# Performance work log

Measured on AMD Instinct MI355X. Metric: run time of the kernel, lower is better.

Reference implementation:

```python
import jax, jax.numpy as jnp
import numpy as np

NUM_HEADS = 4
LOCAL_RADIUS = 2


def setup_inputs() -> dict:
    key = jax.random.key(0)
    ks = jax.random.split(key, 7)
    B, C, H, W = 1, 256, 40, 40
    O = 256  # out_channels
    s = 1.0 / np.sqrt(C).astype(np.float32)
    x = jax.random.normal(ks[0], (B, C, H, W), dtype=jnp.float32)
    Wq = jax.random.normal(ks[1], (C, O), dtype=jnp.float32) * s
    Wk = jax.random.normal(ks[2], (C, O), dtype=jnp.float32) * s
    Wv = jax.random.normal(ks[3], (C, O), dtype=jnp.float32) * s
    bq = jnp.zeros((O,), jnp.float32)
    bk = jnp.zeros((O,), jnp.float32)
    bv = jnp.zeros((O,), jnp.float32)
    return {"x": x, "Wq": Wq, "bq": bq, "Wk": Wk, "bk": bk, "Wv": Wv, "bv": bv}


def reference(x, Wq, bq, Wk, bk, Wv, bv):
    B, C, H, W = x.shape
    N = H * W
    O = Wq.shape[1]
    hd = O // NUM_HEADS
    # Faithful to torch: x.view(B, N, -1) is a raw row-major reshape of (B,C,H,W)
    xf = x.reshape(B, N, C)
    # projections -> (B, heads, N, head_dim)
    q = (xf @ Wq + bq).reshape(B, N, NUM_HEADS, hd).transpose(0, 2, 1, 3)
    k = (xf @ Wk + bk).reshape(B, N, NUM_HEADS, hd).transpose(0, 2, 1, 3)
    v = (xf @ Wv + bv).reshape(B, N, NUM_HEADS, hd).transpose(0, 2, 1, 3)
    scale = jnp.asarray(O, jnp.float32) ** 0.5
    acc = jnp.zeros_like(v)
    # 25 shifted full-attention passes; roll is over (heads, points) axes,
    # exactly matching torch key.roll(shifts=(h,w), dims=(-3,-2)).
    for h in range(-LOCAL_RADIUS, LOCAL_RADIUS + 1):
        for w in range(-LOCAL_RADIUS, LOCAL_RADIUS + 1):
            rk = jnp.roll(k, shift=(h, w), axis=(1, 2))
            scores = jnp.einsum('bhnd,bhmd->bhnm', q, rk) / scale  # (B,h,N,N)
            attn = jax.nn.softmax(scores, axis=-1)
            rv = jnp.roll(v, shift=(-h, -w), axis=(1, 2))
            acc = acc + jnp.einsum('bhnm,bhmd->bhnd', attn, rv)
    # (B, heads, N, hd) -> (B, N, O)
    return acc.transpose(0, 2, 1, 3).reshape(B, N, O)
```

## Files before the change

### kernel.cpp

```cpp
#include <hip/hip_runtime.h>
#include <hip/hip_bf16.h>
#include <stdint.h>

typedef __attribute__((ext_vector_type(8))) __bf16 bf16x8;
typedef __attribute__((ext_vector_type(4))) float f32x4;

#define N_PTS 1600
#define HD    64

#define OFF_XC   0u
#define OFF_WT   819200u
#define OFF_BIAS 1212416u
#define OFF_VHT  1213952u
#define OFF_QH   2033152u
#define OFF_KH   2852352u
#define OFF_KF   0u
#define OFF_OP   2852352u
#define OFF_LP   9405952u
#define OFF_VF   9610752u

__device__ __forceinline__ float bf2f(ushort h) {
  union { uint32_t u; float f; } v; v.u = ((uint32_t)h) << 16; return v.f;
}
__device__ __forceinline__ ushort f2bf(float f) {
  union { float f; uint32_t u; } v; v.f = f;
  uint32_t u = v.u;
  return (ushort)((u + 0x7FFFu + ((u >> 16) & 1u)) >> 16);
}
__device__ __forceinline__ uint32_t pk2(float a, float b) {
  union { __hip_bfloat162 h; uint32_t u; } cv;
  cv.h = __float22bfloat162_rn(make_float2(a, b));
  return cv.u;
}

__device__ __forceinline__ int detect_f32(const ushort* xu, int* shflag) {
  int t = threadIdx.x & 255;
  if (t == 0) *shflag = 0;
  __syncthreads();
  int local = 0;
#pragma unroll
  for (int i = 0; i < 4; ++i) {
    float v = bf2f(xu[(t * 4 + i) * 2]);
    if (!(fabsf(v) < 1e4f)) local = 1;
  }
  if (local) atomicOr(shflag, 1);
  __syncthreads();
  return *shflag;
}

__global__ void k_prep(const void* __restrict__ x, const void* __restrict__ Wq,
                       const void* __restrict__ bq, const void* __restrict__ Wk,
                       const void* __restrict__ bk, const void* __restrict__ Wv,
                       const void* __restrict__ bv, char* __restrict__ ws) {
  __shared__ int shflag;
  __shared__ ushort tileb[32][33];
  int isf32 = detect_f32((const ushort*)x, &shflag);
  int b = blockIdx.x, t = threadIdx.x;

  if (b < 400) {
    ushort4 o;
    if (isf32) {
      float4 f = ((const float4*)x)[b * 256 + t];
      o.x = f2bf(f.x); o.y = f2bf(f.y); o.z = f2bf(f.z); o.w = f2bf(f.w);
    } else {
      o = ((const ushort4*)x)[b * 256 + t];
    }
    ((ushort4*)(ws + OFF_XC))[b * 256 + t] = o;
  } else if (b < 592) {
    int w = b - 400, z = w >> 6, tile = w & 63;
    const void* W = (z == 0) ? Wq : ((z == 1) ? Wk : Wv);
    int o0 = (tile & 7) * 32, k0 = (tile >> 3) * 32;
    int tx = t & 31, ty = t >> 5;
#pragma unroll
    for (int i = 0; i < 32; i += 8) {
      int kk = (k0 + ty + i) * 256 + o0 + tx;
      tileb[ty + i][tx] = isf32 ? f2bf(((const float*)W)[kk]) : ((const ushort*)W)[kk];
    }
    __syncthreads();
    ushort* WT = (ushort*)(ws + OFF_WT) + z * 65536;
#pragma unroll
    for (int i = 0; i < 32; i += 8)
      WT[(o0 + ty + i) * 256 + k0 + tx] = tileb[tx][ty + i];
  } else {
    ushort* bb = (ushort*)(ws + OFF_BIAS);
#pragma unroll
    for (int z = 0; z < 3; ++z) {
      const void* B = (z == 0) ? bq : ((z == 1) ? bk : bv);
      bb[z * 256 + t] = isf32 ? f2bf(((const float*)B)[t]) : ((const ushort*)B)[t];
    }
  }
}

__launch_bounds__(256)
__global__ void k_proj(const ushort* __restrict__ X, const ushort* __restrict__ WT,
                       const ushort* __restrict__ bias3,
                       ushort* __restrict__ Qh, ushort* __restrict__ Kh, ushort* __restrict__ VhT) {
  int z = blockIdx.z;
  const ushort* WTz = WT + z * 65536;
  const ushort* bias = bias3 + z * 256;
  int n0 = blockIdx.x * 16;
  int head = threadIdx.x >> 6;
  int lane = threadIdx.x & 63;
  int c = lane & 15, quad = lane >> 4;

  f32x4 acc[4];
#pragma unroll
  for (int i = 0; i < 4; ++i) acc[i] = (f32x4){0.f, 0.f, 0.f, 0.f};

  const ushort* xrow = X + (n0 + c) * 256;
#pragma unroll
  for (int kt = 0; kt < 8; ++kt) {
    bf16x8 a = *(const bf16x8*)(xrow + kt * 32 + quad * 8);
#pragma unroll
    for (int os = 0; os < 4; ++os) {
      bf16x8 bfr = *(const bf16x8*)(WTz + (head * 64 + os * 16 + c) * 256 + kt * 32 + quad * 8);
      acc[os] = __builtin_amdgcn_mfma_f32_16x16x32_bf16(a, bfr, acc[os], 0, 0, 0);
    }
  }
  if (z == 2) {
#pragma unroll
    for (int os = 0; os < 4; ++os) {
      float bval = bf2f(bias[head * 64 + os * 16 + c]);
      ushort4 v;
      v.x = f2bf(acc[os][0] + bval); v.y = f2bf(acc[os][1] + bval);
      v.z = f2bf(acc[os][2] + bval); v.w = f2bf(acc[os][3] + bval);
      *(ushort4*)(VhT + (head * 64 + os * 16 + c) * N_PTS + n0 + quad * 4) = v;
    }
  } else {
    float scale = (z == 0) ? 0.0625f * 1.44269504088896f : 1.0f;
    ushort* out = (z == 0) ? Qh : Kh;
#pragma unroll
    for (int os = 0; os < 4; ++os) {
      float bval = bf2f(bias[head * 64 + os * 16 + c]);
#pragma unroll
      for (int r = 0; r < 4; ++r)
        out[head * (N_PTS * HD) + (n0 + quad * 4 + r) * HD + os * 16 + c] =
            f2bf((acc[os][r] + bval) * scale);
    }
  }
}

__global__ void k_frag(const ushort* __restrict__ Kh, const ushort* __restrict__ VhT,
                       ushort* __restrict__ Kf, ushort* __restrict__ Vf) {
  int q = blockIdx.x * 256 + threadIdx.x;
  int isV = q >= 51200;
  int idx = isV ? q - 51200 : q;
  int lane = idx & 63, ch = (idx >> 6) & 3;
  int rest = idx >> 8;
  int t = rest % 50, g = rest / 50;
  int c = lane & 15, quad = lane >> 4;
  if (!isV) {
    int perm = ((c >> 2) << 3) + (c & 3);
    int key = t * 32 + perm + ((ch >> 1) << 2);
    int d0 = (ch & 1) * 32 + quad * 8;
    bf16x8 v = *(const bf16x8*)(Kh + (size_t)(g * N_PTS + key) * HD + d0);
    *(bf16x8*)(Kf + (size_t)idx * 8) = v;
  } else {
    int d = ch * 16 + c;
    int m0 = t * 32 + quad * 8;
    const ushort* row = VhT + (size_t)(g * HD + d) * N_PTS;
    int mp = (m0 == 0) ? 1592 : m0 - 8;
    int mn = (m0 == 1592) ? 0 : m0 + 8;
    union { bf16x8 v[3]; ushort us[24]; } w;
    w.v[0] = *(const bf16x8*)(row + mp);
    w.v[1] = *(const bf16x8*)(row + m0);
    w.v[2] = *(const bf16x8*)(row + mn);
    union { ushort us[8]; bf16x8 v; } o;
#pragma unroll
    for (int j = 0; j < 8; ++j) {
      float s = bf2f(w.us[4 + j]) + bf2f(w.us[6 + j]) + bf2f(w.us[8 + j]) +
                bf2f(w.us[10 + j]) + bf2f(w.us[12 + j]);
      o.us[j] = f2bf(s);
    }
    *(bf16x8*)(Vf + (size_t)idx * 8) = o.v;
  }
}

__device__ __forceinline__ bf16x8 pack_p8(const f32x4& s0, const f32x4& s1, float& lp) {
  float e0 = exp2f(s0[0]), e1 = exp2f(s0[1]), e2 = exp2f(s0[2]), e3 = exp2f(s0[3]);
  float e4 = exp2f(s1[0]), e5 = exp2f(s1[1]), e6 = exp2f(s1[2]), e7 = exp2f(s1[3]);
  lp += ((e0 + e1) + (e2 + e3)) + ((e4 + e5) + (e6 + e7));
  union { uint32_t u[4]; bf16x8 v; } r;
  r.u[0] = pk2(e0, e1); r.u[1] = pk2(e2, e3);
  r.u[2] = pk2(e4, e5); r.u[3] = pk2(e6, e7);
  return r.v;
}

__launch_bounds__(256, 4)
__global__ void k_attn(const ushort* __restrict__ Qh, const ushort* __restrict__ Kf,
                       const ushort* __restrict__ Vf, ushort* __restrict__ Opart,
                       float* __restrict__ Lpart) {
  int qt = blockIdx.x;
  int yy = blockIdx.y;
  int z  = blockIdx.z;
  int hp = yy >> 2, kg = yy & 3;
  int vg = (2 * hp - kg + 8) & 3;
  int tid = threadIdx.x, sp = tid >> 6, lane = tid & 63;
  int c = lane & 15, quad = lane >> 4;
  int n0 = qt * 16;

  __shared__ float obuf[4][16][68];
  __shared__ float lbuf[4][16];

  const ushort* q0row = Qh + ((hp    ) * N_PTS + n0 + c) * HD;
  const ushort* q1row = Qh + ((hp + 2) * N_PTS + n0 + c) * HD;
  bf16x8 qa00 = *(const bf16x8*)(q0row + quad * 8);
  bf16x8 qa01 = *(const bf16x8*)(q0row + 32 + quad * 8);
  bf16x8 qa10 = *(const bf16x8*)(q1row + quad * 8);
  bf16x8 qa11 = *(const bf16x8*)(q1row + 32 + quad * 8);

  f32x4 oacc0[4], oacc1[4];
#pragma unroll
  for (int i = 0; i < 4; ++i) {
    oacc0[i] = (f32x4){0.f, 0.f, 0.f, 0.f};
    oacc1[i] = (f32x4){0.f, 0.f, 0.f, 0.f};
  }
  float lp0 = 0.f, lp1 = 0.f;

  int off = (sp == 0) ? 0 : (sp == 1) ? 7 : (sp == 2) ? 13 : 19;
  int iters = (sp == 0) ? 7 : 6;
  int t0 = z * 25 + off;
  const f32x4 z4 = (f32x4){0.f, 0.f, 0.f, 0.f};

  const char* kfp = (const char*)Kf + (size_t)(kg * 50 + t0) * 4096 + lane * 16;
  const char* vfp = (const char*)Vf + (size_t)(vg * 50 + t0) * 4096 + lane * 16;

  for (int it = 0; it < iters; ++it) {
    const char* kt = kfp + it * 4096;
    const char* vt = vfp + it * 4096;
    bf16x8 ka0 = *(const bf16x8*)(kt);
    bf16x8 ka1 = *(const bf16x8*)(kt + 1024);
    bf16x8 kb0 = *(const bf16x8*)(kt + 2048);
    bf16x8 kb1 = *(const bf16x8*)(kt + 3072);
    bf16x8 vb[4];
#pragma unroll
    for (int ds = 0; ds < 4; ++ds)
      vb[ds] = *(const bf16x8*)(vt + ds * 1024);

    f32x4 s0 = __builtin_amdgcn_mfma_f32_16x16x32_bf16(ka0, qa00, z4, 0, 0, 0);
    s0 = __builtin_amdgcn_mfma_f32_16x16x32_bf16(ka1, qa01, s0, 0, 0, 0);
    f32x4 s1 = __builtin_amdgcn_mfma_f32_16x16x32_bf16(kb0, qa00, z4, 0, 0, 0);
    s1 = __builtin_amdgcn_mfma_f32_16x16x32_bf16(kb1, qa01, s1, 0, 0, 0);
    bf16x8 pa = pack_p8(s0, s1, lp0);
#pragma unroll
    for (int ds = 0; ds < 4; ++ds)
      oacc0[ds] = __builtin_amdgcn_mfma_f32_16x16x32_bf16(pa, vb[ds], oacc0[ds], 0, 0, 0);

    s0 = __builtin_amdgcn_mfma_f32_16x16x32_bf16(ka0, qa10, z4, 0, 0, 0);
    s0 = __builtin_amdgcn_mfma_f32_16x16x32_bf16(ka1, qa11, s0, 0, 0, 0);
    s1 = __builtin_amdgcn_mfma_f32_16x16x32_bf16(kb0, qa10, z4, 0, 0, 0);
    s1 = __builtin_amdgcn_mfma_f32_16x16x32_bf16(kb1, qa11, s1, 0, 0, 0);
    bf16x8 pa1 = pack_p8(s0, s1, lp1);
#pragma unroll
    for (int ds = 0; ds < 4; ++ds)
      oacc1[ds] = __builtin_amdgcn_mfma_f32_16x16x32_bf16(pa1, vb[ds], oacc1[ds], 0, 0, 0);
  }

  lp0 += __shfl_xor(lp0, 16, 64); lp0 += __shfl_xor(lp0, 32, 64);
  lp1 += __shfl_xor(lp1, 16, 64); lp1 += __shfl_xor(lp1, 32, 64);

#pragma unroll
  for (int h = 0; h < 2; ++h) {
    __syncthreads();
    const f32x4* oa = h ? oacc1 : oacc0;
#pragma unroll
    for (int ds = 0; ds < 4; ++ds)
#pragma unroll
      for (int r = 0; r < 4; ++r)
        obuf[sp][quad * 4 + r][ds * 16 + c] = oa[ds][r];
    if (quad == 0) lbuf[sp][c] = h ? lp1 : lp0;
    __syncthreads();

    int q = tid >> 4, d0 = (tid & 15) * 4;
    f32x4 a = *(const f32x4*)&obuf[0][q][d0];
    a += *(const f32x4*)&obuf[1][q][d0];
    a += *(const f32x4*)&obuf[2][q][d0];
    a += *(const f32x4*)&obuf[3][q][d0];
    float l = lbuf[0][q] + lbuf[1][q] + lbuf[2][q] + lbuf[3][q];
    int hq = hp + 2 * h;
    union { uint32_t u[2]; } wv;
    wv.u[0] = pk2(a[0], a[1]);
    wv.u[1] = pk2(a[2], a[3]);
    *(uint2*)&Opart[(size_t)((z * 4 + kg) * N_PTS + n0 + q) * 256 + hq * 64 + d0] =
        *(uint2*)wv.u;
    if ((tid & 15) == 0)
      Lpart[((z * 4 + kg) * 4 + hq) * N_PTS + n0 + q] = l;
  }
}

__global__ void k_out(const ushort* __restrict__ Opart, const float* __restrict__ Lpart,
                      const void* __restrict__ x, void* __restrict__ out) {
  __shared__ int shflag;
  int isf32 = detect_f32((const ushort*)x, &shflag);
  int idx = blockIdx.x * 256 + threadIdx.x;
  int n = idx >> 8, o = idx & 255, hq = o >> 6;
  float acc = 0.f;
#pragma unroll
  for (int kg = 0; kg < 4; ++kg) {
    float num = bf2f(Opart[(size_t)((0 + kg) * N_PTS + n) * 256 + o]) +
                bf2f(Opart[(size_t)((4 + kg) * N_PTS + n) * 256 + o]);
    float l = Lpart[((0 + kg) * 4 + hq) * N_PTS + n] +
              Lpart[((4 + kg) * 4 + hq) * N_PTS + n];
    float w = (kg == ((hq + 2) & 3)) ? 2.f : 1.f;
    acc += w * num / l;
  }
  if (isf32) ((float*)out)[idx] = acc;
  else       ((ushort*)out)[idx] = f2bf(acc);
}

extern "C" void kernel_launch(void* const* d_in, const int* in_sizes, int n_in,
                              void* d_out, int out_size, void* d_ws, size_t ws_size,
                              hipStream_t stream) {
  char* ws = (char*)d_ws;
  ushort* Xc    = (ushort*)(ws + OFF_XC);
  ushort* WT    = (ushort*)(ws + OFF_WT);
  ushort* bias3 = (ushort*)(ws + OFF_BIAS);
  ushort* VhT   = (ushort*)(ws + OFF_VHT);
  ushort* Qh    = (ushort*)(ws + OFF_QH);
  ushort* Kh    = (ushort*)(ws + OFF_KH);
  ushort* Kf    = (ushort*)(ws + OFF_KF);
  ushort* Vf    = (ushort*)(ws + OFF_VF);
  ushort* Opart = (ushort*)(ws + OFF_OP);
  float*  Lpart = (float*)(ws + OFF_LP);

  k_prep<<<593, 256, 0, stream>>>(d_in[0], d_in[1], d_in[2], d_in[3],
                                  d_in[4], d_in[5], d_in[6], ws);
  k_proj<<<dim3(100, 1, 3), 256, 0, stream>>>(Xc, WT, bias3, Qh, Kh, VhT);
  k_frag<<<400, 256, 0, stream>>>(Kh, VhT, Kf, Vf);
  k_attn<<<dim3(100, 8, 2), 256, 0, stream>>>(Qh, Kf, Vf, Opart, Lpart);
  k_out<<<1600, 256, 0, stream>>>(Opart, Lpart, d_in[0], d_out);
}
```

Measured before the change: 113.0 us.

## Merge key-split grid dimension and double-buffer K/V fragment loads in attention

Removes the z split of the key range, so each block's four waves now cover all 50 key tiles, and halves the partial outputs that k_out must reduce. The inner loop is rewritten with two register sets (A/B), so the next tile's K/V fragments are loaded while the current tile's MFMAs run. The MFMA sections are wrapped in s_setprio, and the launch_bounds occupancy hint is dropped. The grid shrinks from 1600 to 800 blocks and register pressure rises, which may reduce occupancy and latency hiding.

```diff
diff --git a/kernel.cpp b/kernel.cpp
--- a/kernel.cpp
+++ b/kernel.cpp
@@ -186,13 +186,50 @@
   return r.v;
 }
 
-__launch_bounds__(256, 4)
+#define MFMA16(a, b, cc) __builtin_amdgcn_mfma_f32_16x16x32_bf16(a, b, cc, 0, 0, 0)
+
+#define LOADT(sfx, t) do {                                            \
+    const char* kt_ = kfp + (size_t)(t) * 4096;                       \
+    const char* vt_ = vfp + (size_t)(t) * 4096;                       \
+    ka0##sfx = *(const bf16x8*)(kt_);                                 \
+    ka1##sfx = *(const bf16x8*)(kt_ + 1024);                          \
+    kb0##sfx = *(const bf16x8*)(kt_ + 2048);                          \
+    kb1##sfx = *(const bf16x8*)(kt_ + 3072);                          \
+    vb0##sfx = *(const bf16x8*)(vt_);                                 \
+    vb1##sfx = *(const bf16x8*)(vt_ + 1024);                          \
+    vb2##sfx = *(const bf16x8*)(vt_ + 2048);                          \
+    vb3##sfx = *(const bf16x8*)(vt_ + 3072);                          \
+  } while (0)
+
+#define COMPUTE(sfx) do {                                             \
+    __builtin_amdgcn_s_setprio(1);                                    \
+    f32x4 s0 = MFMA16(ka0##sfx, qa00, z4);                            \
+    s0 = MFMA16(ka1##sfx, qa01, s0);                                  \
+    f32x4 s1 = MFMA16(kb0##sfx, qa00, z4);                            \
+    s1 = MFMA16(kb1##sfx, qa01, s1);                                  \
+    bf16x8 pa0 = pack_p8(s0, s1, lp0);                                \
+    oacc0[0] = MFMA16(pa0, vb0##sfx, oacc0[0]);                       \
+    oacc0[1] = MFMA16(pa0, vb1##sfx, oacc0[1]);                       \
+    oacc0[2] = MFMA16(pa0, vb2##sfx, oacc0[2]);                       \
+    oacc0[3] = MFMA16(pa0, vb3##sfx, oacc0[3]);                       \
+    s0 = MFMA16(ka0##sfx, qa10, z4);                                  \
+    s0 = MFMA16(ka1##sfx, qa11, s0);                                  \
+    s1 = MFMA16(kb0##sfx, qa10, z4);                                  \
+    s1 = MFMA16(kb1##sfx, qa11, s1);                                  \
+    bf16x8 pa1 = pack_p8(s0, s1, lp1);                                \
+    oacc1[0] = MFMA16(pa1, vb0##sfx, oacc1[0]);                       \
+    oacc1[1] = MFMA16(pa1, vb1##sfx, oacc1[1]);                       \
+    oacc1[2] = MFMA16(pa1, vb2##sfx, oacc1[2]);                       \
+    oacc1[3] = MFMA16(pa1, vb3##sfx, oacc1[3]);                       \
+    __builtin_amdgcn_s_setprio(0);                                    \
+  } while (0)
+
+__launch_bounds__(256)
 __global__ void k_attn(const ushort* __restrict__ Qh, const ushort* __restrict__ Kf,
                        const ushort* __restrict__ Vf, ushort* __restrict__ Opart,
                        float* __restrict__ Lpart) {
   int qt = blockIdx.x;
   int yy = blockIdx.y;
-  int z  = blockIdx.z;
   int hp = yy >> 2, kg = yy & 3;
   int vg = (2 * hp - kg + 8) & 3;
   int tid = threadIdx.x, sp = tid >> 6, lane = tid & 63;
@@ -217,44 +254,26 @@
   }
   float lp0 = 0.f, lp1 = 0.f;
 
-  int off = (sp == 0) ? 0 : (sp == 1) ? 7 : (sp == 2) ? 13 : 19;
-  int iters = (sp == 0) ? 7 : 6;
-  int t0 = z * 25 + off;
+  int off = (sp == 0) ? 0 : (sp == 1) ? 13 : (sp == 2) ? 26 : 38;
+  int iters = (sp < 2) ? 13 : 12;
   const f32x4 z4 = (f32x4){0.f, 0.f, 0.f, 0.f};
 
-  const char* kfp = (const char*)Kf + (size_t)(kg * 50 + t0) * 4096 + lane * 16;
-  const char* vfp = (const char*)Vf + (size_t)(vg * 50 + t0) * 4096 + lane * 16;
-
-  for (int it = 0; it < iters; ++it) {
-    const char* kt = kfp + it * 4096;
-    const char* vt = vfp + it * 4096;
-    bf16x8 ka0 = *(const bf16x8*)(kt);
-    bf16x8 ka1 = *(const bf16x8*)(kt + 1024);
-    bf16x8 kb0 = *(const bf16x8*)(kt + 2048);
-    bf16x8 kb1 = *(const bf16x8*)(kt + 3072);
-    bf16x8 vb[4];
-#pragma unroll
-    for (int ds = 0; ds < 4; ++ds)
-      vb[ds] = *(const bf16x8*)(vt + ds * 1024);
-
-    f32x4 s0 = __builtin_amdgcn_mfma_f32_16x16x32_bf16(ka0, qa00, z4, 0, 0, 0);
-    s0 = __builtin_amdgcn_mfma_f32_16x16x32_bf16(ka1, qa01, s0, 0, 0, 0);
-    f32x4 s1 = __builtin_amdgcn_mfma_f32_16x16x32_bf16(kb0, qa00, z4, 0, 0, 0);
-    s1 = __builtin_amdgcn_mfma_f32_16x16x32_bf16(kb1, qa01, s1, 0, 0, 0);
-    bf16x8 pa = pack_p8(s0, s1, lp0);
-#pragma unroll
-    for (int ds = 0; ds < 4; ++ds)
-      oacc0[ds] = __builtin_amdgcn_mfma_f32_16x16x32_bf16(pa, vb[ds], oacc0[ds], 0, 0, 0);
-
-    s0 = __builtin_amdgcn_mfma_f32_16x16x32_bf16(ka0, qa10, z4, 0, 0, 0);
-    s0 = __builtin_amdgcn_mfma_f32_16x16x32_bf16(ka1, qa11, s0, 0, 0, 0);
-    s1 = __builtin_amdgcn_mfma_f32_16x16x32_bf16(kb0, qa10, z4, 0, 0, 0);
-    s1 = __builtin_amdgcn_mfma_f32_16x16x32_bf16(kb1, qa11, s1, 0, 0, 0);
-    bf16x8 pa1 = pack_p8(s0, s1, lp1);
-#pragma unroll
-    for (int ds = 0; ds < 4; ++ds)
-      oacc1[ds] = __builtin_amdgcn_mfma_f32_16x16x32_bf16(pa1, vb[ds], oacc1[ds], 0, 0, 0);
-  }
+  const char* kfp = (const char*)Kf + (size_t)(kg * 50 + off) * 4096 + lane * 16;
+  const char* vfp = (const char*)Vf + (size_t)(vg * 50 + off) * 4096 + lane * 16;
+
+  bf16x8 ka0A, ka1A, kb0A, kb1A, vb0A, vb1A, vb2A, vb3A;
+  bf16x8 ka0B, ka1B, kb0B, kb1B, vb0B, vb1B, vb2B, vb3B;
+
+  LOADT(A, 0);
+  int it = 0;
+  for (; it + 2 <= iters; it += 2) {
+    LOADT(B, it + 1);
+    COMPUTE(A);
+    int tn = (it + 2 < iters) ? (it + 2) : (it + 1);
+    LOADT(A, tn);
+    COMPUTE(B);
+  }
+  if (it < iters) COMPUTE(A);
 
   lp0 += __shfl_xor(lp0, 16, 64); lp0 += __shfl_xor(lp0, 32, 64);
   lp1 += __shfl_xor(lp1, 16, 64); lp1 += __shfl_xor(lp1, 32, 64);
@@ -281,10 +300,10 @@
     union { uint32_t u[2]; } wv;
     wv.u[0] = pk2(a[0], a[1]);
     wv.u[1] = pk2(a[2], a[3]);
-    *(uint2*)&Opart[(size_t)((z * 4 + kg) * N_PTS + n0 + q) * 256 + hq * 64 + d0] =
+    *(uint2*)&Opart[(size_t)(kg * N_PTS + n0 + q) * 256 + hq * 64 + d0] =
         *(uint2*)wv.u;
     if ((tid & 15) == 0)
-      Lpart[((z * 4 + kg) * 4 + hq) * N_PTS + n0 + q] = l;
+      Lpart[(kg * 4 + hq) * N_PTS + n0 + q] = l;
   }
 }
 
@@ -297,10 +316,8 @@
   float acc = 0.f;
 #pragma unroll
   for (int kg = 0; kg < 4; ++kg) {
-    float num = bf2f(Opart[(size_t)((0 + kg) * N_PTS + n) * 256 + o]) +
-                bf2f(Opart[(size_t)((4 + kg) * N_PTS + n) * 256 + o]);
-    float l = Lpart[((0 + kg) * 4 + hq) * N_PTS + n] +
-              Lpart[((4 + kg) * 4 + hq) * N_PTS + n];
+    float num = bf2f(Opart[(size_t)(kg * N_PTS + n) * 256 + o]);
+    float l = Lpart[(kg * 4 + hq) * N_PTS + n];
     float w = (kg == ((hq + 2) & 3)) ? 2.f : 1.f;
     acc += w * num / l;
   }
@@ -327,6 +344,6 @@
                                   d_in[4], d_in[5], d_in[6], ws);
   k_proj<<<dim3(100, 1, 3), 256, 0, stream>>>(Xc, WT, bias3, Qh, Kh, VhT);
   k_frag<<<400, 256, 0, stream>>>(Kh, VhT, Kf, Vf);
-  k_attn<<<dim3(100, 8, 2), 256, 0, stream>>>(Qh, Kf, Vf, Opart, Lpart);
+  k_attn<<<dim3(100, 8), 256, 0, stream>>>(Qh, Kf, Vf, Opart, Lpart);
   k_out<<<1600, 256, 0, stream>>>(Opart, Lpart, d_in[0], d_out);
 }
```

Result: slower. 116.6 us (+3.2%).
